# Kernel optimization log

Measured on AMD Instinct MI355X. Metric: run time of the kernel, lower is better.

The kernel has to match this reference:

```python
import jax, jax.numpy as jnp
import numpy as np


def setup_inputs() -> dict:
    key = jax.random.key(0)
    k1, k2 = jax.random.split(key)
    B, d, h = 65536, 256, 1024  # na = d//4 = 64, G = B//na = 1024, h = 4*d
    x = jax.random.normal(k1, (B, d), dtype=jnp.float32)
    A = 0.1 * jax.random.normal(k2, (d, h), dtype=jnp.float32)
    return {"x": x, "A": A}


def reference(x, A):
    # x: [B, d], A: [d, h] with h = 4*d, na = d // 4, G = B // na
    B, d = x.shape
    na = d // 4
    G = B // na
    n2 = 2 * na

    # bmm with broadcast A + SiLU -> [B, h]; reshape [B, 16, na], sum -> [B]
    J = jax.nn.silu(x @ A)                      # [B, h]
    j12 = J.reshape(B, 16, na).sum(axis=(1, 2)).reshape(G, na)  # [G, na]

    # kron(diag(j12), eye(2)) duplicates each diagonal entry onto a 2x2 identity
    diagvals = jnp.repeat(j12, 2, axis=1)        # [G, 2*na]

    # Final block matrix [[J11, J12], [J21, J22]] with J11=J22=0,
    # J12 = +diag, J21 = -diag, each expanded by kron with eye(2).
    idx = jnp.arange(n2)
    out = jnp.zeros((G, 4 * na, 4 * na), dtype=x.dtype)
    out = out.at[:, idx, n2 + idx].set(diagvals)    # top-right block diagonal
    out = out.at[:, n2 + idx, idx].set(-diagvals)   # bottom-left block diagonal
    return out
```

## Files before the change

kernel.cpp:

```cpp
#include <hip/hip_runtime.h>
#include <stdint.h>

typedef float    f32x4  __attribute__((ext_vector_type(4)));
typedef __bf16   bf16x8 __attribute__((ext_vector_type(8)));
typedef uint32_t u32x4  __attribute__((ext_vector_type(4)));
typedef unsigned short u16x4 __attribute__((ext_vector_type(4)));

#define AS1 __attribute__((address_space(1)))
#define AS3 __attribute__((address_space(3)))

__device__ __forceinline__ unsigned short f2bf_bits(float f) {
  uint32_t u = __builtin_bit_cast(uint32_t, f);
  u += 0x7fffu + ((u >> 16) & 1u);
  return (unsigned short)(u >> 16);
}

__global__ void k_transpose_cvt(const float* __restrict__ A,
                                unsigned short* __restrict__ At) {
  int n = blockIdx.x * blockDim.x + threadIdx.x;
  int o = n << 2;
  int col = o >> 8;
  int k   = o & 255;
  u16x4 v;
#pragma unroll
  for (int j = 0; j < 4; ++j) v[j] = f2bf_bits(A[(size_t)(k + j) * 1024 + col]);
  *reinterpret_cast<u16x4*>(At + o) = v;
}

__launch_bounds__(256, 1)
__global__ void k_fused(const float* __restrict__ x,
                        const unsigned short* __restrict__ At,
                        float* __restrict__ out) {
  __shared__ alignas(16) char lds[4][4][8192];

  const int tid  = threadIdx.x;
  const int lane = tid & 63;
  const int w    = tid >> 6;
  const int g    = blockIdx.x * 4 + w;

  const int col = lane & 15;
  const int hi  = lane >> 4;

  uint32_t soff[8];
#pragma unroll
  for (int i = 0; i < 8; ++i) {
    uint32_t p = (uint32_t)(i * 1024 + lane * 16);
    soff[i] = p ^ (((p >> 9) & 7u) << 4);
  }

#pragma unroll
  for (int t = 0; t < 3; ++t) {
    const char* src = (const char*)At + (size_t)t * 8192;
    char* dst = lds[w][t];
#pragma unroll
    for (int i = 0; i < 8; ++i)
      __builtin_amdgcn_global_load_lds((const AS1 uint32_t*)(src + soff[i]),
                                       (AS3 uint32_t*)(dst + i * 1024), 16, 0, 0);
  }
  __builtin_amdgcn_sched_barrier(0);

  bf16x8 xf[4][8];
#pragma unroll
  for (int r = 0; r < 4; ++r) {
    const float* xr = x + (size_t)(g * 64 + r * 16 + col) * 256;
#pragma unroll
    for (int s = 0; s < 8; ++s) {
      f32x4 a = __builtin_nontemporal_load(
          reinterpret_cast<const f32x4*>(xr + s * 32 + hi * 8));
      f32x4 bq = __builtin_nontemporal_load(
          reinterpret_cast<const f32x4*>(xr + s * 32 + hi * 8 + 4));
      bf16x8 f;
      f[0] = (__bf16)a[0];  f[1] = (__bf16)a[1];
      f[2] = (__bf16)a[2];  f[3] = (__bf16)a[3];
      f[4] = (__bf16)bq[0]; f[5] = (__bf16)bq[1];
      f[6] = (__bf16)bq[2]; f[7] = (__bf16)bq[3];
      xf[r][s] = f;
    }
  }
  asm volatile("s_waitcnt vmcnt(0)" ::: "memory");

  uint32_t rbase = ((uint32_t)(col * 512 + hi * 16)) ^ ((uint32_t)(col & 7) << 4);

  float sums[4][4] = {{0.f,0.f,0.f,0.f},{0.f,0.f,0.f,0.f},
                      {0.f,0.f,0.f,0.f},{0.f,0.f,0.f,0.f}};
  float* og = out + (size_t)g * 65536;
  const f32x4 z4 = {0.f, 0.f, 0.f, 0.f};

  for (int t = 0; t < 64; ++t) {
    asm volatile("s_waitcnt lgkmcnt(0)" ::: "memory");
    {
      int pt = (t + 3) & 63;
      const char* src = (const char*)At + (size_t)pt * 8192;
      char* dst = lds[w][(t + 3) & 3];
#pragma unroll
      for (int i = 0; i < 8; ++i)
        __builtin_amdgcn_global_load_lds((const AS1 uint32_t*)(src + soff[i]),
                                         (AS3 uint32_t*)(dst + i * 1024), 16, 0, 0);
    }
    __builtin_amdgcn_sched_barrier(0);
    {
      float* zp = og + t * 1024 + lane * 4;
#pragma unroll
      for (int q = 0; q < 4; ++q)
        __builtin_nontemporal_store(z4, reinterpret_cast<f32x4*>(zp + q * 256));
    }
    asm volatile("s_waitcnt vmcnt(40)" ::: "memory");

    const char* buf = lds[w][t & 3];
    bf16x8 bfr[8];
#pragma unroll
    for (int s = 0; s < 8; ++s) {
      uint32_t addr = rbase ^ ((uint32_t)s << 6);
      bfr[s] = __builtin_bit_cast(
          bf16x8, *reinterpret_cast<const u32x4*>(buf + addr));
    }
    f32x4 acc[4] = {{0.f,0.f,0.f,0.f},{0.f,0.f,0.f,0.f},
                    {0.f,0.f,0.f,0.f},{0.f,0.f,0.f,0.f}};
#pragma unroll
    for (int s = 0; s < 8; ++s) {
#pragma unroll
      for (int r = 0; r < 4; ++r)
        acc[r] = __builtin_amdgcn_mfma_f32_16x16x32_bf16(xf[r][s], bfr[s],
                                                         acc[r], 0, 0, 0);
    }
#pragma unroll
    for (int r = 0; r < 4; ++r)
#pragma unroll
      for (int j = 0; j < 4; ++j) {
        float z = acc[r][j];
        float sig = __builtin_amdgcn_rcpf(1.0f + __expf(-z));
        sums[r][j] += z * sig;
      }
  }

  asm volatile("s_waitcnt vmcnt(0)" ::: "memory");

#pragma unroll
  for (int r = 0; r < 4; ++r)
#pragma unroll
    for (int j = 0; j < 4; ++j) {
      float v = sums[r][j];
      v += __shfl_xor(v, 1, 64);
      v += __shfl_xor(v, 2, 64);
      v += __shfl_xor(v, 4, 64);
      v += __shfl_xor(v, 8, 64);
      sums[r][j] = v;
    }

  if (col == 0) {
#pragma unroll
    for (int r = 0; r < 4; ++r)
#pragma unroll
      for (int j = 0; j < 4; ++j) {
        int c = r * 16 + hi * 4 + j;
        float s = sums[r][j];
        og[(2 * c) * 256 + 128 + 2 * c]     =  s;
        og[(2 * c + 1) * 256 + 129 + 2 * c] =  s;
        og[(128 + 2 * c) * 256 + 2 * c]     = -s;
        og[(129 + 2 * c) * 256 + 2 * c + 1] = -s;
      }
  }
}

extern "C" void kernel_launch(void* const* d_in, const int* in_sizes, int n_in,
                              void* d_out, int out_size, void* d_ws, size_t ws_size,
                              hipStream_t stream) {
  const float* x = (const float*)d_in[0];
  const float* A = (const float*)d_in[1];
  float* out = (float*)d_out;
  unsigned short* At = (unsigned short*)d_ws;

  k_transpose_cvt<<<256, 256, 0, stream>>>(A, At);
  k_fused<<<256, 256, 0, stream>>>(x, At, out);
}
```

Before: 78.19 us.

## Share A tiles across waves in LDS and split each group over two waves

Each block now handles two groups instead of four, and two waves split each group's 64 rows. The A-tile LDS ring is shared by all four waves, which load it cooperatively and synchronise with s_barrier, instead of each wave holding its own 4-deep copy. The prefetch depth drops from 3 to 2 stages, LDS use falls to 32KB, and the grid doubles to 512 blocks with launch bounds allowing two blocks per CU. The aim is higher occupancy and parallelism with less redundant A traffic, at the cost of per-iteration block barriers and a shallower prefetch. MFMA accumulation is also split into two independent chains per row tile to shorten dependencies.

New measurement: 82.05 us. +4.9%, slower.

```diff
diff --git a/kernel.cpp b/kernel.cpp
--- a/kernel.cpp
+++ b/kernel.cpp
@@ -27,42 +27,42 @@
   *reinterpret_cast<u16x4*>(At + o) = v;
 }
 
-__launch_bounds__(256, 1)
+__launch_bounds__(256, 2)
 __global__ void k_fused(const float* __restrict__ x,
                         const unsigned short* __restrict__ At,
                         float* __restrict__ out) {
-  __shared__ alignas(16) char lds[4][4][8192];
+  __shared__ alignas(16) char lds[4][8192];
 
   const int tid  = threadIdx.x;
   const int lane = tid & 63;
   const int w    = tid >> 6;
-  const int g    = blockIdx.x * 4 + w;
+  const int h    = w & 1;
+  const int g    = blockIdx.x * 2 + (w >> 1);
 
   const int col = lane & 15;
   const int hi  = lane >> 4;
 
-  uint32_t soff[8];
-#pragma unroll
-  for (int i = 0; i < 8; ++i) {
-    uint32_t p = (uint32_t)(i * 1024 + lane * 16);
-    soff[i] = p ^ (((p >> 9) & 7u) << 4);
-  }
+  uint32_t p0  = (uint32_t)((w * 2 + 0) * 1024 + lane * 16);
+  uint32_t so0 = p0 ^ (((p0 >> 9) & 7u) << 4);
+  uint32_t p1  = (uint32_t)((w * 2 + 1) * 1024 + lane * 16);
+  uint32_t so1 = p1 ^ (((p1 >> 9) & 7u) << 4);
+  const uint32_t d0 = (uint32_t)(w * 2 + 0) * 1024;
+  const uint32_t d1 = (uint32_t)(w * 2 + 1) * 1024;
 
 #pragma unroll
-  for (int t = 0; t < 3; ++t) {
+  for (int t = 0; t < 2; ++t) {
     const char* src = (const char*)At + (size_t)t * 8192;
-    char* dst = lds[w][t];
-#pragma unroll
-    for (int i = 0; i < 8; ++i)
-      __builtin_amdgcn_global_load_lds((const AS1 uint32_t*)(src + soff[i]),
-                                       (AS3 uint32_t*)(dst + i * 1024), 16, 0, 0);
+    __builtin_amdgcn_global_load_lds((const AS1 uint32_t*)(src + so0),
+                                     (AS3 uint32_t*)(lds[t] + d0), 16, 0, 0);
+    __builtin_amdgcn_global_load_lds((const AS1 uint32_t*)(src + so1),
+                                     (AS3 uint32_t*)(lds[t] + d1), 16, 0, 0);
   }
   __builtin_amdgcn_sched_barrier(0);
 
-  bf16x8 xf[4][8];
+  bf16x8 xf[2][8];
 #pragma unroll
-  for (int r = 0; r < 4; ++r) {
-    const float* xr = x + (size_t)(g * 64 + r * 16 + col) * 256;
+  for (int r = 0; r < 2; ++r) {
+    const float* xr = x + (size_t)(g * 64 + h * 32 + r * 16 + col) * 256;
 #pragma unroll
     for (int s = 0; s < 8; ++s) {
       f32x4 a = __builtin_nontemporal_load(
@@ -77,36 +77,34 @@
       xf[r][s] = f;
     }
   }
-  asm volatile("s_waitcnt vmcnt(0)" ::: "memory");
+  asm volatile("s_waitcnt vmcnt(0)\n\ts_barrier" ::: "memory");
 
   uint32_t rbase = ((uint32_t)(col * 512 + hi * 16)) ^ ((uint32_t)(col & 7) << 4);
 
-  float sums[4][4] = {{0.f,0.f,0.f,0.f},{0.f,0.f,0.f,0.f},
-                      {0.f,0.f,0.f,0.f},{0.f,0.f,0.f,0.f}};
+  float sums[2][4] = {{0.f,0.f,0.f,0.f},{0.f,0.f,0.f,0.f}};
   float* og = out + (size_t)g * 65536;
+  float* fillbase = og + (size_t)h * 32768 + lane * 4;
   const f32x4 z4 = {0.f, 0.f, 0.f, 0.f};
 
   for (int t = 0; t < 64; ++t) {
-    asm volatile("s_waitcnt lgkmcnt(0)" ::: "memory");
     {
-      int pt = (t + 3) & 63;
+      int pt = (t + 2) & 63;
       const char* src = (const char*)At + (size_t)pt * 8192;
-      char* dst = lds[w][(t + 3) & 3];
-#pragma unroll
-      for (int i = 0; i < 8; ++i)
-        __builtin_amdgcn_global_load_lds((const AS1 uint32_t*)(src + soff[i]),
-                                         (AS3 uint32_t*)(dst + i * 1024), 16, 0, 0);
+      char* dst = lds[(t + 2) & 3];
+      __builtin_amdgcn_global_load_lds((const AS1 uint32_t*)(src + so0),
+                                       (AS3 uint32_t*)(dst + d0), 16, 0, 0);
+      __builtin_amdgcn_global_load_lds((const AS1 uint32_t*)(src + so1),
+                                       (AS3 uint32_t*)(dst + d1), 16, 0, 0);
     }
     __builtin_amdgcn_sched_barrier(0);
     {
-      float* zp = og + t * 1024 + lane * 4;
-#pragma unroll
-      for (int q = 0; q < 4; ++q)
-        __builtin_nontemporal_store(z4, reinterpret_cast<f32x4*>(zp + q * 256));
+      float* zp = fillbase + t * 512;
+      __builtin_nontemporal_store(z4, reinterpret_cast<f32x4*>(zp));
+      __builtin_nontemporal_store(z4, reinterpret_cast<f32x4*>(zp + 256));
     }
-    asm volatile("s_waitcnt vmcnt(40)" ::: "memory");
+    asm volatile("s_waitcnt vmcnt(10)\n\ts_barrier" ::: "memory");
 
-    const char* buf = lds[w][t & 3];
+    const char* buf = lds[t & 3];
     bf16x8 bfr[8];
 #pragma unroll
     for (int s = 0; s < 8; ++s) {
@@ -114,29 +112,30 @@
       bfr[s] = __builtin_bit_cast(
           bf16x8, *reinterpret_cast<const u32x4*>(buf + addr));
     }
-    f32x4 acc[4] = {{0.f,0.f,0.f,0.f},{0.f,0.f,0.f,0.f},
-                    {0.f,0.f,0.f,0.f},{0.f,0.f,0.f,0.f}};
+    f32x4 a00 = {0.f,0.f,0.f,0.f}, a01 = {0.f,0.f,0.f,0.f};
+    f32x4 a10 = {0.f,0.f,0.f,0.f}, a11 = {0.f,0.f,0.f,0.f};
 #pragma unroll
-    for (int s = 0; s < 8; ++s) {
-#pragma unroll
-      for (int r = 0; r < 4; ++r)
-        acc[r] = __builtin_amdgcn_mfma_f32_16x16x32_bf16(xf[r][s], bfr[s],
-                                                         acc[r], 0, 0, 0);
+    for (int s = 0; s < 4; ++s) {
+      a00 = __builtin_amdgcn_mfma_f32_16x16x32_bf16(xf[0][s],     bfr[s],     a00, 0, 0, 0);
+      a01 = __builtin_amdgcn_mfma_f32_16x16x32_bf16(xf[0][s + 4], bfr[s + 4], a01, 0, 0, 0);
+      a10 = __builtin_amdgcn_mfma_f32_16x16x32_bf16(xf[1][s],     bfr[s],     a10, 0, 0, 0);
+      a11 = __builtin_amdgcn_mfma_f32_16x16x32_bf16(xf[1][s + 4], bfr[s + 4], a11, 0, 0, 0);
     }
 #pragma unroll
-    for (int r = 0; r < 4; ++r)
-#pragma unroll
-      for (int j = 0; j < 4; ++j) {
-        float z = acc[r][j];
-        float sig = __builtin_amdgcn_rcpf(1.0f + __expf(-z));
-        sums[r][j] += z * sig;
-      }
+    for (int j = 0; j < 4; ++j) {
+      float z0 = a00[j] + a01[j];
+      float z1 = a10[j] + a11[j];
+      float s0 = __builtin_amdgcn_rcpf(1.0f + __expf(-z0));
+      float s1 = __builtin_amdgcn_rcpf(1.0f + __expf(-z1));
+      sums[0][j] += z0 * s0;
+      sums[1][j] += z1 * s1;
+    }
   }
 
-  asm volatile("s_waitcnt vmcnt(0)" ::: "memory");
+  asm volatile("s_waitcnt vmcnt(0)\n\ts_barrier" ::: "memory");
 
 #pragma unroll
-  for (int r = 0; r < 4; ++r)
+  for (int r = 0; r < 2; ++r)
 #pragma unroll
     for (int j = 0; j < 4; ++j) {
       float v = sums[r][j];
@@ -149,10 +148,10 @@
 
   if (col == 0) {
 #pragma unroll
-    for (int r = 0; r < 4; ++r)
+    for (int r = 0; r < 2; ++r)
 #pragma unroll
       for (int j = 0; j < 4; ++j) {
-        int c = r * 16 + hi * 4 + j;
+        int c = h * 32 + r * 16 + hi * 4 + j;
         float s = sums[r][j];
         og[(2 * c) * 256 + 128 + 2 * c]     =  s;
         og[(2 * c + 1) * 256 + 129 + 2 * c] =  s;
@@ -171,5 +170,5 @@
   unsigned short* At = (unsigned short*)d_ws;
 
   k_transpose_cvt<<<256, 256, 0, stream>>>(A, At);
-  k_fused<<<256, 256, 0, stream>>>(x, At, out);
+  k_fused<<<512, 256, 0, stream>>>(x, At, out);
 }
```

## Split each group's h-dimension across two waves and double the grid

Applied to the files above, without the earlier changes.

Each group of 64 rows is now handled by two waves, each covering half of the 64 A tiles and half of the zero-fill output. Partial sums are combined through shared memory after a block barrier, and each wave writes one off-diagonal block. LDS staging drops from quad to double buffering and launch bounds allow two blocks per CU, so the 512-block grid gives more resident waves to overlap the large zero-fill stores. The costs are that each x tile is loaded twice, the prefetch depth is shallower, and a sync plus LDS reduction is added.

Result: no change. 78.47 us (+0.4%).

```diff
diff --git a/kernel.cpp b/kernel.cpp
--- a/kernel.cpp
+++ b/kernel.cpp
@@ -27,16 +27,18 @@
   *reinterpret_cast<u16x4*>(At + o) = v;
 }
 
-__launch_bounds__(256, 1)
+__launch_bounds__(256, 2)
 __global__ void k_fused(const float* __restrict__ x,
                         const unsigned short* __restrict__ At,
                         float* __restrict__ out) {
-  __shared__ alignas(16) char lds[4][4][8192];
+  __shared__ alignas(16) char lds[4][2][8192];
+  __shared__ float sarr[4][64];
 
   const int tid  = threadIdx.x;
   const int lane = tid & 63;
   const int w    = tid >> 6;
-  const int g    = blockIdx.x * 4 + w;
+  const int th   = w & 1;
+  const int g    = blockIdx.x * 2 + (w >> 1);
 
   const int col = lane & 15;
   const int hi  = lane >> 4;
@@ -48,15 +50,16 @@
     soff[i] = p ^ (((p >> 9) & 7u) << 4);
   }
 
-#pragma unroll
-  for (int t = 0; t < 3; ++t) {
-    const char* src = (const char*)At + (size_t)t * 8192;
-    char* dst = lds[w][t];
+  auto stage = [&](int T) {
+    const char* src = (const char*)At + (size_t)T * 8192;
+    char* dst = lds[w][T & 1];
 #pragma unroll
     for (int i = 0; i < 8; ++i)
       __builtin_amdgcn_global_load_lds((const AS1 uint32_t*)(src + soff[i]),
                                        (AS3 uint32_t*)(dst + i * 1024), 16, 0, 0);
-  }
+  };
+
+  stage(th * 32);
   __builtin_amdgcn_sched_barrier(0);
 
   bf16x8 xf[4][8];
@@ -65,10 +68,8 @@
     const float* xr = x + (size_t)(g * 64 + r * 16 + col) * 256;
 #pragma unroll
     for (int s = 0; s < 8; ++s) {
-      f32x4 a = __builtin_nontemporal_load(
-          reinterpret_cast<const f32x4*>(xr + s * 32 + hi * 8));
-      f32x4 bq = __builtin_nontemporal_load(
-          reinterpret_cast<const f32x4*>(xr + s * 32 + hi * 8 + 4));
+      f32x4 a  = *reinterpret_cast<const f32x4*>(xr + s * 32 + hi * 8);
+      f32x4 bq = *reinterpret_cast<const f32x4*>(xr + s * 32 + hi * 8 + 4);
       bf16x8 f;
       f[0] = (__bf16)a[0];  f[1] = (__bf16)a[1];
       f[2] = (__bf16)a[2];  f[3] = (__bf16)a[3];
@@ -84,29 +85,10 @@
   float sums[4][4] = {{0.f,0.f,0.f,0.f},{0.f,0.f,0.f,0.f},
                       {0.f,0.f,0.f,0.f},{0.f,0.f,0.f,0.f}};
   float* og = out + (size_t)g * 65536;
+  float* fillbase = og + (size_t)th * 32768 + lane * 4;
   const f32x4 z4 = {0.f, 0.f, 0.f, 0.f};
 
-  for (int t = 0; t < 64; ++t) {
-    asm volatile("s_waitcnt lgkmcnt(0)" ::: "memory");
-    {
-      int pt = (t + 3) & 63;
-      const char* src = (const char*)At + (size_t)pt * 8192;
-      char* dst = lds[w][(t + 3) & 3];
-#pragma unroll
-      for (int i = 0; i < 8; ++i)
-        __builtin_amdgcn_global_load_lds((const AS1 uint32_t*)(src + soff[i]),
-                                         (AS3 uint32_t*)(dst + i * 1024), 16, 0, 0);
-    }
-    __builtin_amdgcn_sched_barrier(0);
-    {
-      float* zp = og + t * 1024 + lane * 4;
-#pragma unroll
-      for (int q = 0; q < 4; ++q)
-        __builtin_nontemporal_store(z4, reinterpret_cast<f32x4*>(zp + q * 256));
-    }
-    asm volatile("s_waitcnt vmcnt(40)" ::: "memory");
-
-    const char* buf = lds[w][t & 3];
+  auto do_tile = [&](const char* buf) {
     bf16x8 bfr[8];
 #pragma unroll
     for (int s = 0; s < 8; ++s) {
@@ -131,7 +113,29 @@
         float sig = __builtin_amdgcn_rcpf(1.0f + __expf(-z));
         sums[r][j] += z * sig;
       }
+  };
+
+  for (int t = 0; t < 31; ++t) {
+    asm volatile("s_waitcnt lgkmcnt(0)" ::: "memory");
+    stage(th * 32 + t + 1);
+    __builtin_amdgcn_sched_barrier(0);
+    {
+      float* zp = fillbase + t * 1024;
+#pragma unroll
+      for (int q = 0; q < 4; ++q)
+        __builtin_nontemporal_store(z4, reinterpret_cast<f32x4*>(zp + q * 256));
+    }
+    asm volatile("s_waitcnt vmcnt(16)" ::: "memory");
+    do_tile(lds[w][t & 1]);
   }
+  {
+    float* zp = fillbase + 31 * 1024;
+#pragma unroll
+    for (int q = 0; q < 4; ++q)
+      __builtin_nontemporal_store(z4, reinterpret_cast<f32x4*>(zp + q * 256));
+  }
+  asm volatile("s_waitcnt vmcnt(8)" ::: "memory");
+  do_tile(lds[w][31 & 1]);
 
   asm volatile("s_waitcnt vmcnt(0)" ::: "memory");
 
@@ -146,19 +150,25 @@
       v += __shfl_xor(v, 8, 64);
       sums[r][j] = v;
     }
-
   if (col == 0) {
 #pragma unroll
     for (int r = 0; r < 4; ++r)
 #pragma unroll
-      for (int j = 0; j < 4; ++j) {
-        int c = r * 16 + hi * 4 + j;
-        float s = sums[r][j];
-        og[(2 * c) * 256 + 128 + 2 * c]     =  s;
-        og[(2 * c + 1) * 256 + 129 + 2 * c] =  s;
-        og[(128 + 2 * c) * 256 + 2 * c]     = -s;
-        og[(129 + 2 * c) * 256 + 2 * c + 1] = -s;
-      }
+      for (int j = 0; j < 4; ++j)
+        sarr[w][r * 16 + hi * 4 + j] = sums[r][j];
+  }
+  __syncthreads();
+
+  {
+    int c = lane;
+    float s = sarr[w][c] + sarr[w ^ 1][c];
+    if (th == 0) {
+      og[(2 * c) * 256 + 128 + 2 * c]     =  s;
+      og[(2 * c + 1) * 256 + 129 + 2 * c] =  s;
+    } else {
+      og[(128 + 2 * c) * 256 + 2 * c]     = -s;
+      og[(129 + 2 * c) * 256 + 2 * c + 1] = -s;
+    }
   }
 }
 
@@ -171,5 +181,5 @@
   unsigned short* At = (unsigned short*)d_ws;
 
   k_transpose_cvt<<<256, 256, 0, stream>>>(A, At);
-  k_fused<<<256, 256, 0, stream>>>(x, At, out);
+  k_fused<<<512, 256, 0, stream>>>(x, At, out);
 }
```
